# Kernel optimization log

Measured on AMD Instinct MI355X. Metric: run time of the kernel, lower is better.

## Reference

```python
import jax, jax.numpy as jnp
import numpy as np

H = 128
R = 14
B = 2048
TYPES = ['operator', 'table', 'column', 'predicate', 'operation', 'literal', 'numeral']
SIZES = {'operator': 100000, 'table': 20000, 'column': 120000, 'predicate': 60000,
         'operation': 100000, 'literal': 50000, 'numeral': 50000}
FEAT = {'operator': 4, 'table': 2, 'column': 10, 'predicate': 4, 'operation': 8,
        'literal': 1, 'numeral': 1}
# (name, src_type, dst_type, num_edges), order matches edge_type_mapping in the torch module
EDGES = [('ei_scannedby', 'table', 'operator', 100000),
         ('ei_pred_filters', 'predicate', 'operator', 100000),
         ('ei_outputby', 'column', 'operator', 100000),
         ('ei_col_connects', 'column', 'operation', 100000),
         ('ei_calledby', 'operator', 'operator', 100000),
         ('ei_op_filters', 'operation', 'operator', 100000),
         ('ei_op_connects', 'operation', 'predicate', 100000),
         ('ei_lit_connects', 'literal', 'operation', 100000),
         ('ei_num_connects', 'numeral', 'operation', 100000),
         ('ei_lit_self', 'literal', 'literal', 50000),
         ('ei_num_self', 'numeral', 'numeral', 50000),
         ('ei_tab_self', 'table', 'table', 20000),
         ('ei_col_self', 'column', 'column', 120000),
         ('ei_pred_self', 'predicate', 'predicate', 60000)]
OFFS = {}
_o = 0
for _t in TYPES:
    OFFS[_t] = _o
    _o += SIZES[_t]
N_TOTAL = _o


def setup_inputs():
    key = jax.random.key(0)
    ks = iter(jax.random.split(key, 64))
    inp = {}
    for t in TYPES:
        inp['x_' + t] = jax.random.normal(next(ks), (SIZES[t], FEAT[t]), jnp.float32)
    for name, s, d, E in EDGES:
        src = jax.random.randint(next(ks), (E,), 0, SIZES[s], jnp.int32)
        dst = jax.random.randint(next(ks), (E,), 0, SIZES[d], jnp.int32)
        inp[name] = jnp.stack([src, dst])
    inp['batch_operator'] = jnp.sort(
        jax.random.randint(next(ks), (SIZES['operator'],), 0, B, jnp.int32))

    def lin_w(k, din, dout):
        s = 1.0 / float(np.sqrt(din))
        return jax.random.uniform(k, (din, dout), jnp.float32, -s, s)

    for t in TYPES:
        inp['W_' + t] = lin_w(next(ks), FEAT[t], H)
        inp['b_' + t] = jnp.zeros((H,), jnp.float32)
    for c in ('c1', 'c2'):
        inp[c + '_root'] = lin_w(next(ks), H, H)
        inp[c + '_rel'] = jax.random.normal(next(ks), (R, H, H), jnp.float32) / float(np.sqrt(H))
        inp[c + '_bias'] = jnp.zeros((H,), jnp.float32)
    inp['n1_g'] = jnp.ones((H,), jnp.float32); inp['n1_b'] = jnp.zeros((H,), jnp.float32)
    inp['n2_g'] = jnp.ones((H,), jnp.float32); inp['n2_b'] = jnp.zeros((H,), jnp.float32)
    inp['W_lin'] = lin_w(next(ks), H, 1)
    inp['b_lin'] = jnp.zeros((1,), jnp.float32)
    return inp


def layer_norm(x, g, b, eps=1e-5):
    mu = jnp.mean(x, axis=-1, keepdims=True)
    var = jnp.var(x, axis=-1, keepdims=True)
    return (x - mu) * jax.lax.rsqrt(var + eps) * g + b


def rgcn(x, rel_edges, w_root, w_rel, bias):
    # PyG RGCNConv: root transform + per-relation gather -> GEMM -> scatter-mean into dst
    out = x @ w_root
    for r, (src, dst) in enumerate(rel_edges):
        msg = x[src] @ w_rel[r]  # [E_r, H]
        agg = jax.ops.segment_sum(msg, dst, num_segments=N_TOTAL)
        cnt = jax.ops.segment_sum(jnp.ones(src.shape, x.dtype), dst, num_segments=N_TOTAL)
        out = out + agg / jnp.maximum(cnt, 1.0)[:, None]
    return out + bias


def reference(x_operator, x_table, x_column, x_predicate, x_operation, x_literal, x_numeral,
              ei_scannedby, ei_pred_filters, ei_outputby, ei_col_connects, ei_calledby,
              ei_op_filters, ei_op_connects, ei_lit_connects, ei_num_connects, ei_lit_self,
              ei_num_self, ei_tab_self, ei_col_self, ei_pred_self, batch_operator,
              W_operator, b_operator, W_table, b_table, W_column, b_column,
              W_predicate, b_predicate, W_operation, b_operation, W_literal, b_literal,
              W_numeral, b_numeral, c1_root, c1_rel, c1_bias, c2_root, c2_rel, c2_bias,
              n1_g, n1_b, n2_g, n2_b, W_lin, b_lin):
    # per-node-type input embedding, then concat in fixed type order
    x = jnp.concatenate([
        x_operator @ W_operator + b_operator,
        x_table @ W_table + b_table,
        x_column @ W_column + b_column,
        x_predicate @ W_predicate + b_predicate,
        x_operation @ W_operation + b_operation,
        x_literal @ W_literal + b_literal,
        x_numeral @ W_numeral + b_numeral], axis=0)
    eis = [ei_scannedby, ei_pred_filters, ei_outputby, ei_col_connects, ei_calledby,
           ei_op_filters, ei_op_connects, ei_lit_connects, ei_num_connects, ei_lit_self,
           ei_num_self, ei_tab_self, ei_col_self, ei_pred_self]
    rel_edges = [(e[0] + OFFS[s], e[1] + OFFS[d]) for e, (_, s, d, _) in zip(eis, EDGES)]
    h = rgcn(x, rel_edges, c1_root, c1_rel, c1_bias)
    h = layer_norm(jax.nn.elu(h), n1_g, n1_b)  # dropout is identity in eval mode
    h = rgcn(h, rel_edges, c2_root, c2_rel, c2_bias)
    h = layer_norm(jax.nn.elu(h), n2_g, n2_b)
    op = h[:SIZES['operator']]  # operator offset is 0
    cnt = jax.ops.segment_sum(jnp.ones((op.shape[0],), op.dtype), batch_operator, num_segments=B)
    pooled = jax.ops.segment_sum(op, batch_operator, num_segments=B) / jnp.maximum(cnt, 1.0)[:, None]
    return (pooled @ W_lin + b_lin)[:, 0]  # [B]
```

## Files before the change

### kernel.cpp

```cpp
#include <hip/hip_runtime.h>
#include <hip/hip_bf16.h>
#include <math.h>

#define HD 128
#define N_OP 100000
#define N_L1 400000
#define NB 2048
#define CNT_TOT 1160000
#define EDG_TOT 1100000

typedef short short8 __attribute__((ext_vector_type(8)));
typedef float floatx4 __attribute__((ext_vector_type(4)));

static const int REL_E[14]    = {100000,100000,100000,100000,100000,100000,100000,100000,100000,50000,50000,20000,120000,60000};
static const int REL_DSZ[14]  = {100000,100000,100000,100000,100000,100000,60000,100000,100000,50000,50000,20000,120000,60000};
static const int CNT_OFF[14]  = {0,100000,200000,300000,400000,500000,600000,660000,760000,860000,910000,960000,980000,1100000};
static const int SRC_T[14] = {1,3,2,2,0,4,4,5,6,5,6,1,2,3};
static const int TF[7]  = {4,2,10,4,8,1,1};
static const size_t AGR_OFF[14] = {0,200000,600000,1600000,2600000,3000000,3800000,4280000,4380000,0,0,4480000,4520000,5720000};
#define AGR_TOT 5960000
static const int RELW[14] = {4,7,12,93,23,28,70,104,106,-1,-1,40,54,79};
static const int RELI[14] = {6,11,22,103,27,36,78,105,107,-1,-1,42,64,83};
static const int ROOTW[5] = {0,38,44,66,85};
static const int ROOTB[5] = {37,43,65,84,108};
#define WL1_ROWS 109

__device__ inline unsigned short f2bf(float f) {
  union { float f; unsigned int u; } v; v.f = f;
  unsigned int r = v.u + 0x7FFF + ((v.u >> 16) & 1);
  return (unsigned short)(r >> 16);
}
__device__ inline float bfu2f(unsigned short u) {
  union { unsigned int i; float f; } v; v.i = ((unsigned int)u) << 16; return v.f;
}

struct CJob { const int* dst; int coff; int E; int blk0; };
struct CPackK { CJob j[12]; int bblk0; const int* batch; float* pcnt; int nop; };

__global__ void count_k(CPackK P, int* __restrict__ ICNT) {
  int b = blockIdx.x;
  if (b >= P.bblk0) {
    int i = (b - P.bblk0) * 256 + threadIdx.x;
    if (i < P.nop) atomicAdd(&P.pcnt[P.batch[i]], 1.0f);
    return;
  }
  int ji = 0;
#pragma unroll
  for (int i = 1; i < 12; ++i) if (b >= P.j[i].blk0) ji = i;
  CJob J = P.j[ji];
  int e = (b - J.blk0) * 256 + threadIdx.x;
  if (e < J.E) atomicAdd(&ICNT[J.coff + J.dst[e]], 1);
}

#define SCAN_BLK 1024
__global__ void scan1(const int* __restrict__ in, int* __restrict__ out,
                      int* __restrict__ bsum, int n) {
  __shared__ int sh[256];
  int t = threadIdx.x;
  int base = blockIdx.x * SCAN_BLK + t * 4;
  int v0 = 0, v1 = 0, v2 = 0, v3 = 0;
  if (base + 3 < n) { int4 q = *(const int4*)&in[base]; v0 = q.x; v1 = q.y; v2 = q.z; v3 = q.w; }
  else {
    if (base < n) v0 = in[base];
    if (base + 1 < n) v1 = in[base + 1];
    if (base + 2 < n) v2 = in[base + 2];
    if (base + 3 < n) v3 = in[base + 3];
  }
  int ts = v0 + v1 + v2 + v3;
  sh[t] = ts; __syncthreads();
  for (int o = 1; o < 256; o <<= 1) {
    int x = (t >= o) ? sh[t - o] : 0;
    __syncthreads();
    sh[t] += x;
    __syncthreads();
  }
  int excl = sh[t] - ts;
  if (base < n) out[base] = excl;
  if (base + 1 < n) out[base + 1] = excl + v0;
  if (base + 2 < n) out[base + 2] = excl + v0 + v1;
  if (base + 3 < n) out[base + 3] = excl + v0 + v1 + v2;
  if (t == 255) bsum[blockIdx.x] = sh[255];
}

__global__ void scan2(int* __restrict__ bs, int nb) {
  __shared__ int sh[256];
  int t = threadIdx.x;
  const int C = 5;
  int v[C]; int ts = 0;
#pragma unroll
  for (int i = 0; i < C; ++i) { int idx = t * C + i; v[i] = (idx < nb) ? bs[idx] : 0; ts += v[i]; }
  sh[t] = ts; __syncthreads();
  for (int o = 1; o < 256; o <<= 1) {
    int x = (t >= o) ? sh[t - o] : 0;
    __syncthreads();
    sh[t] += x;
    __syncthreads();
  }
  int run = sh[t] - ts;
#pragma unroll
  for (int i = 0; i < C; ++i) { int idx = t * C + i; if (idx < nb) bs[idx] = run; run += v[i]; }
}

__global__ void scan3(int* __restrict__ CUR, int2* __restrict__ OFF2,
                      const int* __restrict__ ICNT, const int* __restrict__ bs, int n) {
  int i = blockIdx.x * 256 + threadIdx.x;
  if (i < n) {
    int o = CUR[i] + bs[i >> 10];
    CUR[i] = o;
    OFF2[i] = make_int2(o, ICNT[i]);
  }
}

struct FJob { const int* src; const int* dst; int coff; int E; int blk0; };
struct FPackK { FJob j[12]; };

__global__ void fill_k(FPackK P, int* __restrict__ CUR, int* __restrict__ EDG) {
  int b = blockIdx.x;
  int ji = 0;
#pragma unroll
  for (int i = 1; i < 12; ++i) if (b >= P.j[i].blk0) ji = i;
  FJob J = P.j[ji];
  int e = (b - J.blk0) * 256 + threadIdx.x;
  if (e < J.E) {
    int pos = atomicAdd(&CUR[J.coff + J.dst[e]], 1);
    EDG[pos] = J.src[e];
  }
}

struct GJob { const float* x; float* agr; int coff; int D; int F; int blk0; };
struct GPack { GJob j[12]; };

template <int F>
__device__ inline void gathF(const float* __restrict__ x, float* __restrict__ agr,
                             const int* __restrict__ EDG, int2 oc, int d) {
  if (oc.y == 0) return;
  float s[F];
#pragma unroll
  for (int f = 0; f < F; ++f) s[f] = 0.f;
  for (int e = 0; e < oc.y; ++e) {
    int si = EDG[oc.x + e];
    const float* xp = &x[(size_t)si * F];
#pragma unroll
    for (int f = 0; f < F; ++f) s[f] += xp[f];
  }
  float rc = 1.0f / (float)oc.y;
  float* ap = &agr[(size_t)d * F];
#pragma unroll
  for (int f = 0; f < F; ++f) ap[f] = s[f] * rc;
}

__global__ void gather_all(GPack P, const int2* __restrict__ OFF2, const int* __restrict__ EDG) {
  int b = blockIdx.x;
  int ji = 0;
#pragma unroll
  for (int i = 1; i < 12; ++i) if (b >= P.j[i].blk0) ji = i;
  GJob J = P.j[ji];
  int d = (b - J.blk0) * 256 + threadIdx.x;
  if (d >= J.D) return;
  int2 oc = OFF2[J.coff + d];
  switch (J.F) {
    case 1:  gathF<1>(J.x, J.agr, EDG, oc, d); break;
    case 2:  gathF<2>(J.x, J.agr, EDG, oc, d); break;
    case 4:  gathF<4>(J.x, J.agr, EDG, oc, d); break;
    case 8:  gathF<8>(J.x, J.agr, EDG, oc, d); break;
    default: gathF<10>(J.x, J.agr, EDG, oc, d); break;
  }
}

struct CombJob { const float* A; const float* bin; const float* Mtx; const float* extra; float* Wout; float* bout; int F; };
struct CombPack { CombJob j[17]; };

__global__ void weights_prep(CombPack P, const float* __restrict__ c2root,
                             const float* __restrict__ c2rel, __hip_bfloat16* __restrict__ Wt) {
  int b = blockIdx.x;
  if (b < 17) {
    if (threadIdx.x >= 128) return;
    CombJob J = P.j[b];
    int c = threadIdx.x;
    for (int f = 0; f <= J.F; ++f) {
      const float* arow = (f < J.F) ? &J.A[f * HD] : J.bin;
      float s = (f < J.F) ? 0.f : (J.extra ? J.extra[c] : 0.f);
      for (int k = 0; k < HD; ++k) s = fmaf(arow[k], J.Mtx[k * HD + c], s);
      if (f < J.F) J.Wout[f * HD + c] = s;
      else J.bout[c] = s;
    }
  } else {
    const int RID[6] = {-1, 0, 1, 2, 4, 5};
    int j = b - 17;
    const float* W = (j == 0) ? c2root : (c2rel + (size_t)RID[j] * HD * HD);
    __hip_bfloat16* o = Wt + (size_t)j * HD * 136;
    for (int i = threadIdx.x; i < HD * HD; i += 256) {
      int k = i >> 7, n = i & 127;
      o[n * 136 + k] = __float2bfloat16(W[i]);
    }
  }
}

struct L1v2 {
  const float* x0; const float* x1; const float* x2; const float* x3; const float* x4;
  const float* AGR; const float* WL1; const int2* OFF2;
  const float* g; const float* b;
  unsigned short* Hb;
};

template <int F>
__device__ inline void ld_rel(float* s, const float* __restrict__ agr,
                              const int2* __restrict__ OFF2, int cb, int row) {
  int cnt = OFF2[cb + row].y;
  if (cnt > 0) {
    const float* ap = &agr[(size_t)row * F];
#pragma unroll
    for (int f = 0; f < F; ++f) s[f] = ap[f];
    s[F] = 1.f;
  } else {
#pragma unroll
    for (int f = 0; f <= F; ++f) s[f] = 0.f;
  }
}

template <int KT>
__device__ inline void l1_dot8(const float* __restrict__ Ls, const float (&s)[KT],
                               int c4, float (&a)[8]) {
  {
    float4 w0 = *(const float4*)&Ls[KT * 128 + c4];
    float4 w1 = *(const float4*)&Ls[KT * 128 + c4 + 64];
    a[0] = w0.x; a[1] = w0.y; a[2] = w0.z; a[3] = w0.w;
    a[4] = w1.x; a[5] = w1.y; a[6] = w1.z; a[7] = w1.w;
  }
#pragma unroll
  for (int k = 0; k < KT; ++k) {
    float4 w0 = *(const float4*)&Ls[k * 128 + c4];
    float4 w1 = *(const float4*)&Ls[k * 128 + c4 + 64];
    a[0] = fmaf(s[k], w0.x, a[0]); a[1] = fmaf(s[k], w0.y, a[1]);
    a[2] = fmaf(s[k], w0.z, a[2]); a[3] = fmaf(s[k], w0.w, a[3]);
    a[4] = fmaf(s[k], w1.x, a[4]); a[5] = fmaf(s[k], w1.y, a[5]);
    a[6] = fmaf(s[k], w1.z, a[6]); a[7] = fmaf(s[k], w1.w, a[7]);
  }
}

__device__ inline void l1_fin8(float (&a)[8], int c4, const float* __restrict__ g,
                               const float* __restrict__ bb,
                               unsigned short* __restrict__ Hb, int orow) {
  float p = 0.f, q = 0.f;
#pragma unroll
  for (int j = 0; j < 8; ++j) {
    a[j] = (a[j] > 0.f) ? a[j] : (expf(a[j]) - 1.f);
    p += a[j]; q += a[j] * a[j];
  }
#pragma unroll
  for (int m = 8; m >= 1; m >>= 1) {
    p += __shfl_xor(p, m, 64);
    q += __shfl_xor(q, m, 64);
  }
  float mean = p * (1.0f / HD);
  float var = q * (1.0f / HD) - mean * mean;
  float rstd = rsqrtf(var + 1e-5f);
  float4 g0 = *(const float4*)&g[c4], g1 = *(const float4*)&g[c4 + 64];
  float4 b0 = *(const float4*)&bb[c4], b1 = *(const float4*)&bb[c4 + 64];
  float gg[8] = {g0.x, g0.y, g0.z, g0.w, g1.x, g1.y, g1.z, g1.w};
  float bv[8] = {b0.x, b0.y, b0.z, b0.w, b1.x, b1.y, b1.z, b1.w};
  float o[8];
#pragma unroll
  for (int j = 0; j < 8; ++j) o[j] = (a[j] - mean) * rstd * gg[j] + bv[j];
  uint2 lo, hi;
  lo.x = (unsigned int)f2bf(o[0]) | ((unsigned int)f2bf(o[1]) << 16);
  lo.y = (unsigned int)f2bf(o[2]) | ((unsigned int)f2bf(o[3]) << 16);
  hi.x = (unsigned int)f2bf(o[4]) | ((unsigned int)f2bf(o[5]) << 16);
  hi.y = (unsigned int)f2bf(o[6]) | ((unsigned int)f2bf(o[7]) << 16);
  *(uint2*)&Hb[(size_t)orow * HD + c4] = lo;
  *(uint2*)&Hb[(size_t)orow * HD + c4 + 64] = hi;
}

__global__ __launch_bounds__(256) void layer1_v4(L1v2 A) {
  __shared__ float Ls[38 * 128];
  const int b = blockIdx.x, t = threadIdx.x;
  const int wv = t >> 6, ln = t & 63;
  const int sub = ln >> 4, c4 = (ln & 15) * 4;
  int type, seg;
  if (b < 1563) { type = 0; seg = b; }
  else if (b < 1876) { type = 1; seg = b - 1563; }
  else if (b < 3751) { type = 2; seg = b - 1876; }
  else if (b < 4689) { type = 3; seg = b - 3751; }
  else { type = 4; seg = b - 4689; }
  const int NR[5] = {38, 6, 22, 19, 24};
  const int RB[5] = {0, 38, 44, 66, 85};
  const int TR[5] = {100000, 20000, 120000, 60000, 100000};
  const int OB[5] = {0, 100000, 120000, 240000, 300000};
  {
    const float4* src = (const float4*)(A.WL1 + RB[type] * 128);
    float4* dst = (float4*)Ls;
    int n4 = NR[type] * 32;
    for (int i = t; i < n4; i += 256) dst[i] = src[i];
  }
  __syncthreads();
  const int row0 = seg * 64, M = TR[type], ob = OB[type];

  if (type == 0) {
#pragma unroll
    for (int it = 0; it < 4; ++it) {
      int row = row0 + it * 16 + wv * 4 + sub;
      if (row >= M) continue;
      float s[37];
      const float* xp = &A.x0[(size_t)row * 4];
#pragma unroll
      for (int f = 0; f < 4; ++f) s[f] = xp[f];
      ld_rel<2>(s + 4, A.AGR + 0, A.OFF2, 0, row);
      ld_rel<4>(s + 7, A.AGR + 200000, A.OFF2, 100000, row);
      ld_rel<10>(s + 12, A.AGR + 600000, A.OFF2, 200000, row);
      ld_rel<4>(s + 23, A.AGR + 2600000, A.OFF2, 400000, row);
      ld_rel<8>(s + 28, A.AGR + 3000000, A.OFF2, 500000, row);
      float a[8];
      l1_dot8<37>(Ls, s, c4, a);
      l1_fin8(a, c4, A.g, A.b, A.Hb, ob + row);
    }
  } else if (type == 1) {
#pragma unroll
    for (int it = 0; it < 4; ++it) {
      int row = row0 + it * 16 + wv * 4 + sub;
      if (row >= M) continue;
      float s[5];
      const float* xp = &A.x1[(size_t)row * 2];
#pragma unroll
      for (int f = 0; f < 2; ++f) s[f] = xp[f];
      ld_rel<2>(s + 2, A.AGR + 4480000, A.OFF2, 960000, row);
      float a[8];
      l1_dot8<5>(Ls, s, c4, a);
      l1_fin8(a, c4, A.g, A.b, A.Hb, ob + row);
    }
  } else if (type == 2) {
#pragma unroll
    for (int it = 0; it < 4; ++it) {
      int row = row0 + it * 16 + wv * 4 + sub;
      if (row >= M) continue;
      float s[21];
      const float* xp = &A.x2[(size_t)row * 10];
#pragma unroll
      for (int f = 0; f < 10; ++f) s[f] = xp[f];
      ld_rel<10>(s + 10, A.AGR + 4520000, A.OFF2, 980000, row);
      float a[8];
      l1_dot8<21>(Ls, s, c4, a);
      l1_fin8(a, c4, A.g, A.b, A.Hb, ob + row);
    }
  } else if (type == 3) {
#pragma unroll
    for (int it = 0; it < 4; ++it) {
      int row = row0 + it * 16 + wv * 4 + sub;
      if (row >= M) continue;
      float s[18];
      const float* xp = &A.x3[(size_t)row * 4];
#pragma unroll
      for (int f = 0; f < 4; ++f) s[f] = xp[f];
      ld_rel<8>(s + 4, A.AGR + 3800000, A.OFF2, 600000, row);
      ld_rel<4>(s + 13, A.AGR + 5720000, A.OFF2, 1100000, row);
      float a[8];
      l1_dot8<18>(Ls, s, c4, a);
      l1_fin8(a, c4, A.g, A.b, A.Hb, ob + row);
    }
  } else {
#pragma unroll
    for (int it = 0; it < 4; ++it) {
      int row = row0 + it * 16 + wv * 4 + sub;
      if (row >= M) continue;
      float s[23];
      const float* xp = &A.x4[(size_t)row * 8];
#pragma unroll
      for (int f = 0; f < 8; ++f) s[f] = xp[f];
      ld_rel<10>(s + 8, A.AGR + 1600000, A.OFF2, 300000, row);
      ld_rel<1>(s + 19, A.AGR + 4280000, A.OFF2, 660000, row);
      ld_rel<1>(s + 21, A.AGR + 4380000, A.OFF2, 760000, row);
      float a[8];
      l1_dot8<23>(Ls, s, c4, a);
      l1_fin8(a, c4, A.g, A.b, A.Hb, ob + row);
    }
  }
}

__global__ __launch_bounds__(256, 4)
void l2_fused(const unsigned short* __restrict__ Hb, const unsigned short* __restrict__ Wall,
              const int2* __restrict__ OFF2, const int* __restrict__ EDG,
              const float* __restrict__ c2bias, const float* __restrict__ n2g,
              const float* __restrict__ n2b, const float* __restrict__ Wl,
              const int* __restrict__ batch, float* __restrict__ accb, int M) {
  const int CSR_OFF[5] = {0, 100000, 200000, 400000, 500000};
  const int SOFF[5]    = {100000, 240000, 120000, 0, 300000};
  __shared__ unsigned short Ws[128 * 136];
  const int t = threadIdx.x, wv = t >> 6, ln = t & 63;
  const int quad = ln >> 4, ln15 = ln & 15, q8 = quad * 8;
  const int m0 = blockIdx.x * 64;
  const int rowA = m0 + wv * 16 + ln15;

  float bias_c[8], gw[8];
  float pg = 0.f, pb = 0.f;
#pragma unroll
  for (int nt = 0; nt < 8; ++nt) {
    int col = nt * 16 + ln15;
    float wl = Wl[col], gc = n2g[col], bc = n2b[col];
    bias_c[nt] = c2bias[col];
    gw[nt] = gc * wl;
    pg += gc * wl;
    pb += bc * wl;
  }
#pragma unroll
  for (int m = 8; m >= 1; m >>= 1) {
    pg += __shfl_xor(pg, m, 64);
    pb += __shfl_xor(pb, m, 64);
  }

  floatx4 acc[8];
#pragma unroll
  for (int b = 0; b < 8; ++b) acc[b] = (floatx4){0.f, 0.f, 0.f, 0.f};

  for (int term = 0; term < 6; ++term) {
    __syncthreads();
    {
      const uint4* wg = (const uint4*)(Wall + (size_t)term * 128 * 136);
      uint4* ws4 = (uint4*)Ws;
#pragma unroll
      for (int i = 0; i < 9; ++i) {
        int idx = i * 256 + t;
        if (idx < 2176) ws4[idx] = wg[idx];
      }
    }
    __syncthreads();

    short8 afr[4];
    if (term == 0) {
      if (rowA < M) {
#pragma unroll
        for (int k4 = 0; k4 < 4; ++k4)
          afr[k4] = *(const short8*)&Hb[(size_t)rowA * HD + k4 * 32 + q8];
      } else {
#pragma unroll
        for (int k4 = 0; k4 < 4; ++k4)
#pragma unroll
          for (int j = 0; j < 8; ++j) afr[k4][j] = 0;
      }
    } else {
      float sum[4][8];
#pragma unroll
      for (int k4 = 0; k4 < 4; ++k4)
#pragma unroll
        for (int j = 0; j < 8; ++j) sum[k4][j] = 0.f;
      if (rowA < M) {
        int2 oc = OFF2[CSR_OFF[term - 1] + rowA];
        if (oc.y > 0) {
          int so = SOFF[term - 1];
          for (int e = 0; e < oc.y; ++e) {
            size_t s = (size_t)(EDG[oc.x + e] + so);
#pragma unroll
            for (int k4 = 0; k4 < 4; ++k4) {
              short8 h = *(const short8*)&Hb[s * HD + k4 * 32 + q8];
#pragma unroll
              for (int j = 0; j < 8; ++j) sum[k4][j] += bfu2f((unsigned short)h[j]);
            }
          }
          float rc = 1.0f / (float)oc.y;
#pragma unroll
          for (int k4 = 0; k4 < 4; ++k4)
#pragma unroll
            for (int j = 0; j < 8; ++j) sum[k4][j] *= rc;
        }
      }
#pragma unroll
      for (int k4 = 0; k4 < 4; ++k4)
#pragma unroll
        for (int j = 0; j < 8; ++j) afr[k4][j] = (short)f2bf(sum[k4][j]);
    }

#pragma unroll
    for (int nt = 0; nt < 8; ++nt) {
      int wrow = nt * 16 + ln15;
      short8 b0 = *(const short8*)&Ws[wrow * 136 + 0 + q8];
      short8 b1 = *(const short8*)&Ws[wrow * 136 + 32 + q8];
      short8 b2 = *(const short8*)&Ws[wrow * 136 + 64 + q8];
      short8 b3 = *(const short8*)&Ws[wrow * 136 + 96 + q8];
      acc[nt] = __builtin_amdgcn_mfma_f32_16x16x32_bf16(afr[0], b0, acc[nt], 0, 0, 0);
      acc[nt] = __builtin_amdgcn_mfma_f32_16x16x32_bf16(afr[1], b1, acc[nt], 0, 0, 0);
      acc[nt] = __builtin_amdgcn_mfma_f32_16x16x32_bf16(afr[2], b2, acc[nt], 0, 0, 0);
      acc[nt] = __builtin_amdgcn_mfma_f32_16x16x32_bf16(afr[3], b3, acc[nt], 0, 0, 0);
    }
  }

#pragma unroll
  for (int r = 0; r < 4; ++r) {
    int rowD = m0 + wv * 16 + quad * 4 + r;
    float p = 0.f, q = 0.f, s1 = 0.f;
#pragma unroll
    for (int nt = 0; nt < 8; ++nt) {
      float v = acc[nt][r] + bias_c[nt];
      float e = (v > 0.f) ? v : (expf(v) - 1.f);
      p += e; q += e * e; s1 += e * gw[nt];
    }
#pragma unroll
    for (int m = 8; m >= 1; m >>= 1) {
      p += __shfl_xor(p, m, 64);
      q += __shfl_xor(q, m, 64);
      s1 += __shfl_xor(s1, m, 64);
    }
    if (ln15 == 0 && rowD < M) {
      float mean = p * (1.0f / HD);
      float var = q * (1.0f / HD) - mean * mean;
      float rstd = rsqrtf(var + 1e-5f);
      float o = rstd * (s1 - mean * pg) + pb;
      atomicAdd(&accb[batch[rowD]], o);
    }
  }
}

__global__ void final_kernel(const float* __restrict__ accb, const float* __restrict__ pcnt,
                             const float* __restrict__ bl, float* __restrict__ out) {
  int b = blockIdx.x * 256 + threadIdx.x;
  if (b < NB) out[b] = accb[b] / fmaxf(pcnt[b], 1.0f) + bl[0];
}

extern "C" void kernel_launch(void* const* d_in, const int* in_sizes, int n_in,
                              void* d_out, int out_size, void* d_ws, size_t ws_size,
                              hipStream_t stream) {
  const float* xt[7];
  for (int t = 0; t < 7; ++t) xt[t] = (const float*)d_in[t];
  const int* ei[14];
  for (int r = 0; r < 14; ++r) ei[r] = (const int*)d_in[7 + r];
  const int* batch = (const int*)d_in[21];
  const float* Wemb[7]; const float* bemb[7];
  for (int t = 0; t < 7; ++t) { Wemb[t] = (const float*)d_in[22 + 2 * t]; bemb[t] = (const float*)d_in[23 + 2 * t]; }
  const float* c_root[2] = {(const float*)d_in[36], (const float*)d_in[39]};
  const float* c_rel[2]  = {(const float*)d_in[37], (const float*)d_in[40]};
  const float* c_bias[2] = {(const float*)d_in[38], (const float*)d_in[41]};
  const float* ng[2] = {(const float*)d_in[42], (const float*)d_in[44]};
  const float* nbv[2] = {(const float*)d_in[43], (const float*)d_in[45]};
  const float* Wlin = (const float*)d_in[46];
  const float* blin = (const float*)d_in[47];
  float* out = (float*)d_out;

  char* base = (char*)d_ws;
  size_t off = 0;
  auto alloc = [&](size_t bytes) -> void* {
    void* p = base + off;
    off += (bytes + 255) & ~(size_t)255;
    return p;
  };
  __hip_bfloat16* Hb = (__hip_bfloat16*)alloc((size_t)N_L1 * HD * 2);
  float* AGR  = (float*)alloc((size_t)AGR_TOT * 4);
  int*   ICNT = (int*)alloc((size_t)CNT_TOT * 4);
  int*   CUR  = (int*)alloc((size_t)CNT_TOT * 4);
  int2*  OFF2 = (int2*)alloc((size_t)CNT_TOT * 8);
  int*   EDG  = (int*)alloc((size_t)EDG_TOT * 4);
  int*   BS   = (int*)alloc((size_t)1152 * 4);
  float* WL1  = (float*)alloc((size_t)WL1_ROWS * 128 * 4);
  __hip_bfloat16* WT2 = (__hip_bfloat16*)alloc((size_t)6 * HD * 136 * 2);
  float* ACC  = (float*)alloc((size_t)NB * 4);
  float* PCNT = (float*)alloc((size_t)NB * 4);

  static const int l1_rels[12] = {0,1,2,3,4,5,6,7,8,11,12,13};

  hipMemsetAsync(ICNT, 0, (size_t)CNT_TOT * 4, stream);
  hipMemsetAsync(ACC, 0, (size_t)2 * NB * 4, stream);

  CPackK CP1;
  int blk = 0;
  for (int q = 0; q < 12; ++q) {
    int r = l1_rels[q];
    CP1.j[q].dst = ei[r] + REL_E[r];
    CP1.j[q].coff = CNT_OFF[r];
    CP1.j[q].E = REL_E[r];
    CP1.j[q].blk0 = blk;
    blk += (REL_E[r] + 255) / 256;
  }
  CP1.bblk0 = blk; CP1.batch = batch; CP1.pcnt = PCNT; CP1.nop = N_OP;
  blk += (N_OP + 255) / 256;
  count_k<<<blk, 256, 0, stream>>>(CP1, ICNT);

  int nb1 = (CNT_TOT + SCAN_BLK - 1) / SCAN_BLK;
  scan1<<<nb1, 256, 0, stream>>>(ICNT, CUR, BS, CNT_TOT);
  scan2<<<1, 256, 0, stream>>>(BS, nb1);
  scan3<<<(CNT_TOT + 255) / 256, 256, 0, stream>>>(CUR, OFF2, ICNT, BS, CNT_TOT);

  FPackK FP;
  blk = 0;
  for (int q = 0; q < 12; ++q) {
    int r = l1_rels[q];
    FP.j[q].src = ei[r];
    FP.j[q].dst = ei[r] + REL_E[r];
    FP.j[q].coff = CNT_OFF[r];
    FP.j[q].E = REL_E[r];
    FP.j[q].blk0 = blk;
    blk += (REL_E[r] + 255) / 256;
  }
  fill_k<<<blk, 256, 0, stream>>>(FP, CUR, EDG);

  CombPack CP;
  for (int q = 0; q < 12; ++q) {
    int r = l1_rels[q]; int t = SRC_T[r];
    CombJob& J = CP.j[q];
    J.A = Wemb[t]; J.bin = bemb[t]; J.Mtx = c_rel[0] + (size_t)r * HD * HD;
    J.extra = nullptr;
    J.Wout = WL1 + (size_t)RELW[r] * 128;
    J.bout = WL1 + (size_t)RELI[r] * 128;
    J.F = TF[t];
  }
  for (int t = 0; t < 5; ++t) {
    CombJob& J = CP.j[12 + t];
    J.A = Wemb[t]; J.bin = bemb[t]; J.Mtx = c_root[0];
    J.extra = c_bias[0];
    J.Wout = WL1 + (size_t)ROOTW[t] * 128;
    J.bout = WL1 + (size_t)ROOTB[t] * 128;
    J.F = TF[t];
  }
  weights_prep<<<23, 256, 0, stream>>>(CP, c_root[1], c_rel[1], WT2);

  GPack GP;
  blk = 0;
  for (int q = 0; q < 12; ++q) {
    int r = l1_rels[q]; int t = SRC_T[r];
    GP.j[q].x = xt[t];
    GP.j[q].agr = AGR + AGR_OFF[r];
    GP.j[q].coff = CNT_OFF[r];
    GP.j[q].D = REL_DSZ[r];
    GP.j[q].F = TF[t];
    GP.j[q].blk0 = blk;
    blk += (REL_DSZ[r] + 255) / 256;
  }
  gather_all<<<blk, 256, 0, stream>>>(GP, OFF2, EDG);

  L1v2 A;
  A.x0 = xt[0]; A.x1 = xt[1]; A.x2 = xt[2]; A.x3 = xt[3]; A.x4 = xt[4];
  A.AGR = AGR; A.WL1 = WL1; A.OFF2 = OFF2;
  A.g = ng[0]; A.b = nbv[0]; A.Hb = (unsigned short*)Hb;
  layer1_v4<<<6252, 256, 0, stream>>>(A);

  l2_fused<<<(N_OP + 63) / 64, 256, 0, stream>>>(
      (const unsigned short*)Hb, (const unsigned short*)WT2,
      OFF2, EDG, c_bias[1], ng[1], nbv[1], Wlin, batch, ACC, N_OP);

  final_kernel<<<(NB + 255) / 256, 256, 0, stream>>>(ACC, PCNT, blin, out);
}
```

Baseline: 604.2 us.

## Double rows per block in layer-2 fused kernel and vectorize layer-1 feature loads

The layer-2 fused kernel now processes 128 rows per block, two 16-row M-tiles per wave. Each weight tile staged in shared memory is reused across twice as many rows, and the CSR offsets are prefetched once up front instead of per term. The occupancy hint drops from 4 to 3 blocks because of the extra accumulator and fragment registers, and the grid halves. Layer 1 switches its scalar feature and aggregate loads to float2/float4 vector loads.

```diff
diff --git a/kernel.cpp b/kernel.cpp
--- a/kernel.cpp
+++ b/kernel.cpp
@@ -203,18 +203,49 @@
   unsigned short* Hb;
 };
 
-template <int F>
-__device__ inline void ld_rel(float* s, const float* __restrict__ agr,
+__device__ inline void ldv2(float* s, const float* __restrict__ p) {
+  float2 v = *(const float2*)p; s[0] = v.x; s[1] = v.y;
+}
+__device__ inline void ldv4(float* s, const float* __restrict__ p) {
+  float4 v = *(const float4*)p; s[0] = v.x; s[1] = v.y; s[2] = v.z; s[3] = v.w;
+}
+__device__ inline void relF1(float* s, const float* __restrict__ agr,
+                             const int2* __restrict__ OFF2, int cb, int row) {
+  if (OFF2[cb + row].y > 0) { s[0] = agr[row]; s[1] = 1.f; }
+  else { s[0] = 0.f; s[1] = 0.f; }
+}
+__device__ inline void relF2(float* s, const float* __restrict__ agr,
+                             const int2* __restrict__ OFF2, int cb, int row) {
+  if (OFF2[cb + row].y > 0) { ldv2(s, &agr[(size_t)row * 2]); s[2] = 1.f; }
+  else { s[0] = s[1] = s[2] = 0.f; }
+}
+__device__ inline void relF4(float* s, const float* __restrict__ agr,
+                             const int2* __restrict__ OFF2, int cb, int row) {
+  if (OFF2[cb + row].y > 0) { ldv4(s, &agr[(size_t)row * 4]); s[4] = 1.f; }
+  else {
+#pragma unroll
+    for (int f = 0; f < 5; ++f) s[f] = 0.f;
+  }
+}
+__device__ inline void relF8(float* s, const float* __restrict__ agr,
+                             const int2* __restrict__ OFF2, int cb, int row) {
+  if (OFF2[cb + row].y > 0) {
+    ldv4(s, &agr[(size_t)row * 8]); ldv4(s + 4, &agr[(size_t)row * 8 + 4]); s[8] = 1.f;
+  } else {
+#pragma unroll
+    for (int f = 0; f < 9; ++f) s[f] = 0.f;
+  }
+}
+__device__ inline void relF10(float* s, const float* __restrict__ agr,
                               const int2* __restrict__ OFF2, int cb, int row) {
-  int cnt = OFF2[cb + row].y;
-  if (cnt > 0) {
-    const float* ap = &agr[(size_t)row * F];
-#pragma unroll
-    for (int f = 0; f < F; ++f) s[f] = ap[f];
-    s[F] = 1.f;
+  if (OFF2[cb + row].y > 0) {
+    const float* p = &agr[(size_t)row * 10];
+#pragma unroll
+    for (int j = 0; j < 5; ++j) ldv2(s + 2 * j, p + 2 * j);
+    s[10] = 1.f;
   } else {
 #pragma unroll
-    for (int f = 0; f <= F; ++f) s[f] = 0.f;
+    for (int f = 0; f < 11; ++f) s[f] = 0.f;
   }
 }
 
@@ -271,7 +302,7 @@
   *(uint2*)&Hb[(size_t)orow * HD + c4 + 64] = hi;
 }
 
-__global__ __launch_bounds__(256) void layer1_v4(L1v2 A) {
+__global__ __launch_bounds__(256) void layer1_v5(L1v2 A) {
   __shared__ float Ls[38 * 128];
   const int b = blockIdx.x, t = threadIdx.x;
   const int wv = t >> 6, ln = t & 63;
@@ -301,14 +332,12 @@
       int row = row0 + it * 16 + wv * 4 + sub;
       if (row >= M) continue;
       float s[37];
-      const float* xp = &A.x0[(size_t)row * 4];
-#pragma unroll
-      for (int f = 0; f < 4; ++f) s[f] = xp[f];
-      ld_rel<2>(s + 4, A.AGR + 0, A.OFF2, 0, row);
-      ld_rel<4>(s + 7, A.AGR + 200000, A.OFF2, 100000, row);
-      ld_rel<10>(s + 12, A.AGR + 600000, A.OFF2, 200000, row);
-      ld_rel<4>(s + 23, A.AGR + 2600000, A.OFF2, 400000, row);
-      ld_rel<8>(s + 28, A.AGR + 3000000, A.OFF2, 500000, row);
+      ldv4(s, &A.x0[(size_t)row * 4]);
+      relF2(s + 4, A.AGR + 0, A.OFF2, 0, row);
+      relF4(s + 7, A.AGR + 200000, A.OFF2, 100000, row);
+      relF10(s + 12, A.AGR + 600000, A.OFF2, 200000, row);
+      relF4(s + 23, A.AGR + 2600000, A.OFF2, 400000, row);
+      relF8(s + 28, A.AGR + 3000000, A.OFF2, 500000, row);
       float a[8];
       l1_dot8<37>(Ls, s, c4, a);
       l1_fin8(a, c4, A.g, A.b, A.Hb, ob + row);
@@ -319,10 +348,8 @@
       int row = row0 + it * 16 + wv * 4 + sub;
       if (row >= M) continue;
       float s[5];
-      const float* xp = &A.x1[(size_t)row * 2];
-#pragma unroll
-      for (int f = 0; f < 2; ++f) s[f] = xp[f];
-      ld_rel<2>(s + 2, A.AGR + 4480000, A.OFF2, 960000, row);
+      ldv2(s, &A.x1[(size_t)row * 2]);
+      relF2(s + 2, A.AGR + 4480000, A.OFF2, 960000, row);
       float a[8];
       l1_dot8<5>(Ls, s, c4, a);
       l1_fin8(a, c4, A.g, A.b, A.Hb, ob + row);
@@ -333,10 +360,10 @@
       int row = row0 + it * 16 + wv * 4 + sub;
       if (row >= M) continue;
       float s[21];
-      const float* xp = &A.x2[(size_t)row * 10];
-#pragma unroll
-      for (int f = 0; f < 10; ++f) s[f] = xp[f];
-      ld_rel<10>(s + 10, A.AGR + 4520000, A.OFF2, 980000, row);
+      const float* p = &A.x2[(size_t)row * 10];
+#pragma unroll
+      for (int j = 0; j < 5; ++j) ldv2(s + 2 * j, p + 2 * j);
+      relF10(s + 10, A.AGR + 4520000, A.OFF2, 980000, row);
       float a[8];
       l1_dot8<21>(Ls, s, c4, a);
       l1_fin8(a, c4, A.g, A.b, A.Hb, ob + row);
@@ -347,11 +374,9 @@
       int row = row0 + it * 16 + wv * 4 + sub;
       if (row >= M) continue;
       float s[18];
-      const float* xp = &A.x3[(size_t)row * 4];
-#pragma unroll
-      for (int f = 0; f < 4; ++f) s[f] = xp[f];
-      ld_rel<8>(s + 4, A.AGR + 3800000, A.OFF2, 600000, row);
-      ld_rel<4>(s + 13, A.AGR + 5720000, A.OFF2, 1100000, row);
+      ldv4(s, &A.x3[(size_t)row * 4]);
+      relF8(s + 4, A.AGR + 3800000, A.OFF2, 600000, row);
+      relF4(s + 13, A.AGR + 5720000, A.OFF2, 1100000, row);
       float a[8];
       l1_dot8<18>(Ls, s, c4, a);
       l1_fin8(a, c4, A.g, A.b, A.Hb, ob + row);
@@ -362,12 +387,11 @@
       int row = row0 + it * 16 + wv * 4 + sub;
       if (row >= M) continue;
       float s[23];
-      const float* xp = &A.x4[(size_t)row * 8];
-#pragma unroll
-      for (int f = 0; f < 8; ++f) s[f] = xp[f];
-      ld_rel<10>(s + 8, A.AGR + 1600000, A.OFF2, 300000, row);
-      ld_rel<1>(s + 19, A.AGR + 4280000, A.OFF2, 660000, row);
-      ld_rel<1>(s + 21, A.AGR + 4380000, A.OFF2, 760000, row);
+      ldv4(s, &A.x4[(size_t)row * 8]);
+      ldv4(s + 4, &A.x4[(size_t)row * 8 + 4]);
+      relF10(s + 8, A.AGR + 1600000, A.OFF2, 300000, row);
+      relF1(s + 19, A.AGR + 4280000, A.OFF2, 660000, row);
+      relF1(s + 21, A.AGR + 4380000, A.OFF2, 760000, row);
       float a[8];
       l1_dot8<23>(Ls, s, c4, a);
       l1_fin8(a, c4, A.g, A.b, A.Hb, ob + row);
@@ -375,7 +399,7 @@
   }
 }
 
-__global__ __launch_bounds__(256, 4)
+__global__ __launch_bounds__(256, 3)
 void l2_fused(const unsigned short* __restrict__ Hb, const unsigned short* __restrict__ Wall,
               const int2* __restrict__ OFF2, const int* __restrict__ EDG,
               const float* __restrict__ c2bias, const float* __restrict__ n2g,
@@ -386,8 +410,16 @@
   __shared__ unsigned short Ws[128 * 136];
   const int t = threadIdx.x, wv = t >> 6, ln = t & 63;
   const int quad = ln >> 4, ln15 = ln & 15, q8 = quad * 8;
-  const int m0 = blockIdx.x * 64;
-  const int rowA = m0 + wv * 16 + ln15;
+  const int m0 = blockIdx.x * 128;
+
+  int2 ocs[2][5];
+#pragma unroll
+  for (int mt = 0; mt < 2; ++mt) {
+    int rowA = m0 + (wv * 2 + mt) * 16 + ln15;
+#pragma unroll
+    for (int r = 0; r < 5; ++r)
+      ocs[mt][r] = (rowA < M) ? OFF2[CSR_OFF[r] + rowA] : make_int2(0, 0);
+  }
 
   float bias_c[8], gw[8];
   float pg = 0.f, pb = 0.f;
@@ -406,9 +438,11 @@
     pb += __shfl_xor(pb, m, 64);
   }
 
-  floatx4 acc[8];
-#pragma unroll
-  for (int b = 0; b < 8; ++b) acc[b] = (floatx4){0.f, 0.f, 0.f, 0.f};
+  floatx4 acc[2][8];
+#pragma unroll
+  for (int a = 0; a < 2; ++a)
+#pragma unroll
+    for (int b = 0; b < 8; ++b) acc[a][b] = (floatx4){0.f, 0.f, 0.f, 0.f};
 
   for (int term = 0; term < 6; ++term) {
     __syncthreads();
@@ -423,26 +457,28 @@
     }
     __syncthreads();
 
-    short8 afr[4];
-    if (term == 0) {
-      if (rowA < M) {
+    short8 afr[2][4];
+#pragma unroll
+    for (int mt = 0; mt < 2; ++mt) {
+      int rowA = m0 + (wv * 2 + mt) * 16 + ln15;
+      if (term == 0) {
+        if (rowA < M) {
+#pragma unroll
+          for (int k4 = 0; k4 < 4; ++k4)
+            afr[mt][k4] = *(const short8*)&Hb[(size_t)rowA * HD + k4 * 32 + q8];
+        } else {
+#pragma unroll
+          for (int k4 = 0; k4 < 4; ++k4)
+#pragma unroll
+            for (int j = 0; j < 8; ++j) afr[mt][k4][j] = 0;
+        }
+      } else {
+        float sum[4][8];
 #pragma unroll
         for (int k4 = 0; k4 < 4; ++k4)
-          afr[k4] = *(const short8*)&Hb[(size_t)rowA * HD + k4 * 32 + q8];
-      } else {
-#pragma unroll
-        for (int k4 = 0; k4 < 4; ++k4)
-#pragma unroll
-          for (int j = 0; j < 8; ++j) afr[k4][j] = 0;
-      }
-    } else {
-      float sum[4][8];
-#pragma unroll
-      for (int k4 = 0; k4 < 4; ++k4)
-#pragma unroll
-        for (int j = 0; j < 8; ++j) sum[k4][j] = 0.f;
-      if (rowA < M) {
-        int2 oc = OFF2[CSR_OFF[term - 1] + rowA];
+#pragma unroll
+          for (int j = 0; j < 8; ++j) sum[k4][j] = 0.f;
+        int2 oc = ocs[mt][term - 1];
         if (oc.y > 0) {
           int so = SOFF[term - 1];
           for (int e = 0; e < oc.y; ++e) {
@@ -460,11 +496,11 @@
 #pragma unroll
             for (int j = 0; j < 8; ++j) sum[k4][j] *= rc;
         }
+#pragma unroll
+        for (int k4 = 0; k4 < 4; ++k4)
+#pragma unroll
+          for (int j = 0; j < 8; ++j) afr[mt][k4][j] = (short)f2bf(sum[k4][j]);
       }
-#pragma unroll
-      for (int k4 = 0; k4 < 4; ++k4)
-#pragma unroll
-        for (int j = 0; j < 8; ++j) afr[k4][j] = (short)f2bf(sum[k4][j]);
     }
 
 #pragma unroll
@@ -474,35 +510,41 @@
       short8 b1 = *(const short8*)&Ws[wrow * 136 + 32 + q8];
       short8 b2 = *(const short8*)&Ws[wrow * 136 + 64 + q8];
       short8 b3 = *(const short8*)&Ws[wrow * 136 + 96 + q8];
-      acc[nt] = __builtin_amdgcn_mfma_f32_16x16x32_bf16(afr[0], b0, acc[nt], 0, 0, 0);
-      acc[nt] = __builtin_amdgcn_mfma_f32_16x16x32_bf16(afr[1], b1, acc[nt], 0, 0, 0);
-      acc[nt] = __builtin_amdgcn_mfma_f32_16x16x32_bf16(afr[2], b2, acc[nt], 0, 0, 0);
-      acc[nt] = __builtin_amdgcn_mfma_f32_16x16x32_bf16(afr[3], b3, acc[nt], 0, 0, 0);
-    }
-  }
-
-#pragma unroll
-  for (int r = 0; r < 4; ++r) {
-    int rowD = m0 + wv * 16 + quad * 4 + r;
-    float p = 0.f, q = 0.f, s1 = 0.f;
-#pragma unroll
-    for (int nt = 0; nt < 8; ++nt) {
-      float v = acc[nt][r] + bias_c[nt];
-      float e = (v > 0.f) ? v : (expf(v) - 1.f);
-      p += e; q += e * e; s1 += e * gw[nt];
-    }
-#pragma unroll
-    for (int m = 8; m >= 1; m >>= 1) {
-      p += __shfl_xor(p, m, 64);
-      q += __shfl_xor(q, m, 64);
-      s1 += __shfl_xor(s1, m, 64);
-    }
-    if (ln15 == 0 && rowD < M) {
-      float mean = p * (1.0f / HD);
-      float var = q * (1.0f / HD) - mean * mean;
-      float rstd = rsqrtf(var + 1e-5f);
-      float o = rstd * (s1 - mean * pg) + pb;
-      atomicAdd(&accb[batch[rowD]], o);
+#pragma unroll
+      for (int mt = 0; mt < 2; ++mt) {
+        acc[mt][nt] = __builtin_amdgcn_mfma_f32_16x16x32_bf16(afr[mt][0], b0, acc[mt][nt], 0, 0, 0);
+        acc[mt][nt] = __builtin_amdgcn_mfma_f32_16x16x32_bf16(afr[mt][1], b1, acc[mt][nt], 0, 0, 0);
+        acc[mt][nt] = __builtin_amdgcn_mfma_f32_16x16x32_bf16(afr[mt][2], b2, acc[mt][nt], 0, 0, 0);
+        acc[mt][nt] = __builtin_amdgcn_mfma_f32_16x16x32_bf16(afr[mt][3], b3, acc[mt][nt], 0, 0, 0);
+      }
+    }
+  }
+
+#pragma unroll
+  for (int mt = 0; mt < 2; ++mt) {
+#pragma unroll
+    for (int r = 0; r < 4; ++r) {
+      int rowD = m0 + (wv * 2 + mt) * 16 + quad * 4 + r;
+      float p = 0.f, q = 0.f, s1 = 0.f;
+#pragma unroll
+      for (int nt = 0; nt < 8; ++nt) {
+        float v = acc[mt][nt][r] + bias_c[nt];
+        float e = (v > 0.f) ? v : (expf(v) - 1.f);
+        p += e; q += e * e; s1 += e * gw[nt];
+      }
+#pragma unroll
+      for (int m = 8; m >= 1; m >>= 1) {
+        p += __shfl_xor(p, m, 64);
+        q += __shfl_xor(q, m, 64);
+        s1 += __shfl_xor(s1, m, 64);
+      }
+      if (ln15 == 0 && rowD < M) {
+        float mean = p * (1.0f / HD);
+        float var = q * (1.0f / HD) - mean * mean;
+        float rstd = rsqrtf(var + 1e-5f);
+        float o = rstd * (s1 - mean * pg) + pb;
+        atomicAdd(&accb[batch[rowD]], o);
+      }
     }
   }
 }
@@ -626,9 +668,9 @@
   A.x0 = xt[0]; A.x1 = xt[1]; A.x2 = xt[2]; A.x3 = xt[3]; A.x4 = xt[4];
   A.AGR = AGR; A.WL1 = WL1; A.OFF2 = OFF2;
   A.g = ng[0]; A.b = nbv[0]; A.Hb = (unsigned short*)Hb;
-  layer1_v4<<<6252, 256, 0, stream>>>(A);
-
-  l2_fused<<<(N_OP + 63) / 64, 256, 0, stream>>>(
+  layer1_v5<<<6252, 256, 0, stream>>>(A);
+
+  l2_fused<<<(N_OP + 127) / 128, 256, 0, stream>>>(
       (const unsigned short*)Hb, (const unsigned short*)WT2,
       OFF2, EDG, c_bias[1], ng[1], nbv[1], Wlin, batch, ACC, N_OP);
 
```

After: 652.5 us. 8.0% more time.
